# Performance work log

Measured on AMD Instinct MI355X. Metric: run time of the kernel, lower is better.

## Reference

```python
import jax, jax.numpy as jnp
import numpy as np

B, T = 4, 2048
OBS, ST = 512, 512
H, E = 8, 64

def setup_inputs() -> dict:
    key = jax.random.key(0)
    k1, k2, k3, k4, k5 = jax.random.split(key, 5)
    observe = jax.random.normal(k1, (B, T, OBS), dtype=jnp.float32)
    state = jax.random.normal(k2, (B, T, ST), dtype=jnp.float32)
    # nn.Linear weights (out, in) applied as x @ W.T; store transposed for einsum
    Wq = jax.random.normal(k3, (OBS, H * E), dtype=jnp.float32) * (1.0 / np.sqrt(OBS))
    Wk = jax.random.normal(k4, (ST, H * E), dtype=jnp.float32) * (1.0 / np.sqrt(ST))
    Wv = jax.random.normal(k5, (ST, H * E), dtype=jnp.float32) * (1.0 / np.sqrt(ST))
    merge_w = jnp.ones((1, H, E), dtype=jnp.float32)  # Merger weight, init fill_(1.0)
    return {"observe": observe, "state": state, "Wq": Wq, "Wk": Wk, "Wv": Wv, "merge_w": merge_w}

def reference(observe, state, Wq, Wk, Wv, merge_w):
    b, t, _ = observe.shape
    h, e = H, E
    scale = e ** 0.25
    q = (observe @ Wq).reshape(b, t, h, e).transpose(0, 2, 1, 3) / scale  # [b,h,t,e]
    k = (state @ Wk).reshape(b, t, h, e).transpose(0, 2, 1, 3) / scale
    v = (state @ Wv).reshape(b, t, h, e).transpose(0, 2, 1, 3)
    dot = jnp.einsum('bhqe,bhke->bhqk', q, k)  # [b,h,t,t]
    attn = jax.nn.softmax(dot, axis=-1)
    out = jnp.einsum('bhqk,bhke->bhqe', attn, v)  # [b,h,t,e]
    out = out.transpose(0, 2, 1, 3).reshape(b * t, h, e)  # [b*t,h,e]
    # Merger: softmax over head dim of learned weight, weighted head sum
    w = jax.nn.softmax(merge_w, axis=1)  # [1,h,e]
    return jnp.sum(w * out, axis=1)  # [b*t,e]
```

## Files before the change

kernel.cpp:

```cpp
#include <hip/hip_runtime.h>

#define B_ 4
#define T_ 2048
#define H_ 8
#define E_ 64
#define KDIM 512

typedef unsigned short ushort_t;
typedef __attribute__((ext_vector_type(4))) float f32x4;
typedef __attribute__((ext_vector_type(4))) int i32x4;
typedef __attribute__((ext_vector_type(8))) short s16x8;

#define QK_SCALE 0.42466043f

__device__ __forceinline__ ushort_t f2bf(float f) {
  unsigned u = __builtin_bit_cast(unsigned, f);
  u += 0x7fffu + ((u >> 16) & 1u);
  return (ushort_t)(u >> 16);
}
__device__ __forceinline__ unsigned pk2(float a, float b) {
  return (unsigned)f2bf(a) | ((unsigned)f2bf(b) << 16);
}
__device__ __forceinline__ unsigned pk2t(float a, float b) {
  return __builtin_amdgcn_perm(__builtin_bit_cast(unsigned, b),
                               __builtin_bit_cast(unsigned, a), 0x07060302u);
}
__device__ __forceinline__ float e2(float x) { return __builtin_amdgcn_exp2f(x); }
__device__ __forceinline__ void gl2lds16(const void* g, void* l) {
  __builtin_amdgcn_global_load_lds((const __attribute__((address_space(1))) unsigned*)g,
                                   (__attribute__((address_space(3))) unsigned*)l, 16, 0, 0);
}

__global__ void k_prep(const float* __restrict__ Wq, const float* __restrict__ Wk,
                       const float* __restrict__ Wv, ushort_t* __restrict__ wt) {
  __shared__ ushort_t tile[64][66];
  int z = blockIdx.z;
  const float* W = (z == 0) ? Wq : (z == 1 ? Wk : Wv);
  float scale = (z < 2) ? QK_SCALE : 1.0f;
  int k0 = blockIdx.y << 6, n0 = blockIdx.x << 6;
  int rr = threadIdx.x >> 6, cc = threadIdx.x & 63;
  for (int p = 0; p < 16; p++) {
    int kl = p * 4 + rr;
    tile[cc][kl] = f2bf(W[(size_t)(k0 + kl) * 512 + n0 + cc] * scale);
  }
  __syncthreads();
  int kp2 = threadIdx.x & 31, nr = threadIdx.x >> 5;
  unsigned* wt32 = (unsigned*)(wt + (size_t)z * 262144);
  for (int p = 0; p < 8; p++) {
    int nl = p * 8 + nr;
    unsigned val = (unsigned)tile[nl][kp2 * 2] | ((unsigned)tile[nl][kp2 * 2 + 1] << 16);
    wt32[(size_t)(n0 + nl) * 256 + (k0 >> 1) + kp2] = val;
  }
}

__global__ void k_wgt(const float* __restrict__ mw, float* __restrict__ wgt) {
  int e = threadIdx.x;
  float w[8], wmax = -1e30f;
  for (int h = 0; h < 8; h++) { w[h] = mw[h * 64 + e]; wmax = fmaxf(wmax, w[h]); }
  float wsum = 0.f;
  for (int h = 0; h < 8; h++) { w[h] = __expf(w[h] - wmax); wsum += w[h]; }
  float inv = 1.f / wsum;
  for (int h = 0; h < 8; h++) wgt[h * 64 + e] = w[h] * inv;
}

__global__ void k_cvt(const float* __restrict__ obs, const float* __restrict__ st,
                      unsigned* __restrict__ xo, unsigned* __restrict__ xs) {
  int which = blockIdx.y;
  const float* src = which ? st : obs;
  unsigned* dst = which ? xs : xo;
  size_t idx = (size_t)blockIdx.x * 256 + threadIdx.x;
  size_t base = idx * 8;
  float4 x0 = *(const float4*)(src + base);
  float4 x1 = *(const float4*)(src + base + 4);
  uint4 d;
  d.x = pk2(x0.x, x0.y);
  d.y = pk2(x0.z, x0.w);
  d.z = pk2(x1.x, x1.y);
  d.w = pk2(x1.z, x1.w);
  *(uint4*)(dst + idx * 4) = d;
}

__global__ __launch_bounds__(256, 3) void k_proj2(
    const ushort_t* __restrict__ xo, const ushort_t* __restrict__ xs,
    const ushort_t* __restrict__ wt,
    ushort_t* __restrict__ qo, ushort_t* __restrict__ ko, ushort_t* __restrict__ vto) {
  __shared__ __align__(16) ushort_t As[3][128 * 64];

  int id = blockIdx.x;
  int xcd = id & 7, nt = (id >> 3) & 3, ghi = id >> 5;
  int g = ghi * 8 + xcd;
  int which = g >> 6, mb = g & 63;
  int m0 = mb << 7, n0 = nt << 7;
  const ushort_t* X = (which == 0) ? xo : xs;
  const ushort_t* W = wt + which * 262144;

  int tid = threadIdx.x, wave = tid >> 6, lane = tid & 63;
  int l15 = lane & 15, quad = lane >> 4;
  int wm = wave & 1, wn = wave >> 1;

  f32x4 acc[4][4];
  for (int i = 0; i < 4; i++)
    for (int j = 0; j < 4; j++) acc[i][j] = (f32x4){0.f, 0.f, 0.f, 0.f};

  int arl = lane >> 3, ap = lane & 7;

#define STAGEA(buf, k0)                                                            \
  do {                                                                             \
    for (int ii = 0; ii < 4; ii++) {                                               \
      int r = wave * 32 + ii * 8 + arl;                                            \
      gl2lds16(X + (size_t)(m0 + r) * KDIM + (k0) + ((ap ^ (r & 7)) << 3),         \
               &As[buf][(wave * 32 + ii * 8) * 64]);                               \
    }                                                                              \
  } while (0)

  const ushort_t* wb[4];
  for (int j = 0; j < 4; j++)
    wb[j] = W + (size_t)(n0 + wn * 64 + j * 16 + l15) * KDIM + quad * 8;

  STAGEA(0, 0);
  STAGEA(1, 64);
  __builtin_amdgcn_s_waitcnt(0x0F74);
  __builtin_amdgcn_s_barrier();
  __builtin_amdgcn_sched_barrier(0);

#pragma unroll
  for (int kt = 0; kt < 8; kt++) {
    s16x8 b[2][4];
    for (int kc = 0; kc < 2; kc++)
      for (int j = 0; j < 4; j++) b[kc][j] = *(const s16x8*)(wb[j] + kc * 32);
    for (int j = 0; j < 4; j++) wb[j] += 64;
    if (kt < 6) STAGEA((kt + 2) % 3, (kt + 2) * 64);
    if (kt < 6) __builtin_amdgcn_s_waitcnt(0x0F74);
    else        __builtin_amdgcn_s_waitcnt(0x0F70);
    __builtin_amdgcn_sched_barrier(0);
    const ushort_t* asb = As[kt % 3];
    for (int kc = 0; kc < 2; kc++) {
      s16x8 a[4];
      for (int i = 0; i < 4; i++) {
        int mr = wm * 64 + i * 16 + l15;
        int pc = (kc * 4 + quad) ^ (l15 & 7);
        a[i] = *(const s16x8*)&asb[mr * 64 + pc * 8];
      }
      if (which == 2) {
        for (int i = 0; i < 4; i++)
          for (int j = 0; j < 4; j++)
            acc[i][j] = __builtin_amdgcn_mfma_f32_16x16x32_bf16(b[kc][j], a[i], acc[i][j], 0, 0, 0);
      } else {
        for (int i = 0; i < 4; i++)
          for (int j = 0; j < 4; j++)
            acc[i][j] = __builtin_amdgcn_mfma_f32_16x16x32_bf16(a[i], b[kc][j], acc[i][j], 0, 0, 0);
      }
    }
    if (kt < 7) {
      __builtin_amdgcn_s_barrier();
      __builtin_amdgcn_sched_barrier(0);
    }
  }
#undef STAGEA

  if (which != 2) {
    ushort_t* dst = (which == 0) ? qo : ko;
    for (int i = 0; i < 4; i++) {
      int grow = m0 + wm * 64 + i * 16 + quad * 4;
      for (int j = 0; j < 4; j++) {
        int gcol = n0 + wn * 64 + j * 16 + l15;
        int h = gcol >> 6, e = gcol & 63;
        for (int r = 0; r < 4; r++) {
          int row = grow + r;
          int bb = row >> 11, t = row & 2047;
          int bh = bb * H_ + h;
          dst[(((size_t)bh * T_ + t) << 6) + e] = f2bf(acc[i][j][r]);
        }
      }
    }
  } else {
    for (int i = 0; i < 4; i++) {
      int row = m0 + wm * 64 + i * 16 + l15;
      int bb = row >> 11, t = row & 2047;
      for (int j = 0; j < 4; j++) {
        for (int r = 0; r < 4; r++) {
          int gcol = n0 + wn * 64 + j * 16 + quad * 4 + r;
          int h = gcol >> 6, e = gcol & 63;
          int bh = bb * H_ + h;
          vto[((size_t)(bh << 6) + e) * T_ + t] = f2bf(acc[i][j][r]);
        }
      }
    }
  }
}

__global__ __launch_bounds__(256, 3) void k_proj(
    const float* __restrict__ obs, const float* __restrict__ st,
    const ushort_t* __restrict__ wt,
    ushort_t* __restrict__ qo, ushort_t* __restrict__ ko, ushort_t* __restrict__ vto) {
  __shared__ __align__(16) float As[2][128 * 32];

  int id = blockIdx.x;
  int xcd = id & 7, nt = (id >> 3) & 3, ghi = id >> 5;
  int g = ghi * 8 + xcd;
  int which = g >> 6, mb = g & 63;
  int m0 = mb << 7, n0 = nt << 7;
  const float* X = (which == 0) ? obs : st;
  const ushort_t* W = wt + which * 262144;

  int tid = threadIdx.x, wave = tid >> 6, lane = tid & 63;
  int l15 = lane & 15, quad = lane >> 4;
  int wm = wave & 1, wn = wave >> 1;

  f32x4 acc[4][4];
  for (int i = 0; i < 4; i++)
    for (int j = 0; j < 4; j++) acc[i][j] = (f32x4){0.f, 0.f, 0.f, 0.f};

  int arl = lane >> 3, ap = lane & 7;

#define STAGEA(buf, k0)                                                           \
  do {                                                                            \
    for (int ii = 0; ii < 4; ii++) {                                              \
      int r = wave * 32 + ii * 8 + arl;                                           \
      gl2lds16(X + (size_t)(m0 + r) * KDIM + (k0) + ((ap ^ (r & 7)) << 2),        \
               &As[buf][(wave * 32 + ii * 8) * 32]);                              \
    }                                                                             \
  } while (0)

  const ushort_t* wb[4];
  for (int j = 0; j < 4; j++)
    wb[j] = W + (size_t)(n0 + wn * 64 + j * 16 + l15) * KDIM + quad * 8;

  STAGEA(0, 0);
  __builtin_amdgcn_s_waitcnt(0x0F70);
  __syncthreads();

  for (int kt = 0; kt < 16; kt++) {
    s16x8 b[4];
    for (int j = 0; j < 4; j++) { b[j] = *(const s16x8*)wb[j]; wb[j] += 32; }
    if (kt < 15) STAGEA((kt + 1) & 1, kt * 32 + 32);
    const float* asb = As[kt & 1];
    s16x8 a[4];
    for (int i = 0; i < 4; i++) {
      int mr = wm * 64 + i * 16 + l15;
      int s = mr & 7;
      const float* rowp = &asb[mr * 32];
      float4 x0 = *(const float4*)&rowp[(((quad << 1)) ^ s) << 2];
      float4 x1 = *(const float4*)&rowp[(((quad << 1) | 1) ^ s) << 2];
      i32x4 d;
      d[0] = (int)pk2(x0.x, x0.y);
      d[1] = (int)pk2(x0.z, x0.w);
      d[2] = (int)pk2(x1.x, x1.y);
      d[3] = (int)pk2(x1.z, x1.w);
      a[i] = __builtin_bit_cast(s16x8, d);
    }
    if (which == 2) {
      for (int i = 0; i < 4; i++)
        for (int j = 0; j < 4; j++)
          acc[i][j] = __builtin_amdgcn_mfma_f32_16x16x32_bf16(b[j], a[i], acc[i][j], 0, 0, 0);
    } else {
      for (int i = 0; i < 4; i++)
        for (int j = 0; j < 4; j++)
          acc[i][j] = __builtin_amdgcn_mfma_f32_16x16x32_bf16(a[i], b[j], acc[i][j], 0, 0, 0);
    }
    __builtin_amdgcn_s_waitcnt(0x0F70);
    __syncthreads();
  }
#undef STAGEA

  if (which != 2) {
    ushort_t* dst = (which == 0) ? qo : ko;
    for (int i = 0; i < 4; i++) {
      int grow = m0 + wm * 64 + i * 16 + quad * 4;
      for (int j = 0; j < 4; j++) {
        int gcol = n0 + wn * 64 + j * 16 + l15;
        int h = gcol >> 6, e = gcol & 63;
        for (int r = 0; r < 4; r++) {
          int row = grow + r;
          int bb = row >> 11, t = row & 2047;
          int bh = bb * H_ + h;
          dst[(((size_t)bh * T_ + t) << 6) + e] = f2bf(acc[i][j][r]);
        }
      }
    }
  } else {
    for (int i = 0; i < 4; i++) {
      int row = m0 + wm * 64 + i * 16 + l15;
      int bb = row >> 11, t = row & 2047;
      for (int j = 0; j < 4; j++) {
        for (int r = 0; r < 4; r++) {
          int gcol = n0 + wn * 64 + j * 16 + quad * 4 + r;
          int h = gcol >> 6, e = gcol & 63;
          int bh = bb * H_ + h;
          vto[((size_t)(bh << 6) + e) * T_ + t] = f2bf(acc[i][j][r]);
        }
      }
    }
  }
}

union AttnSmem {
  struct { ushort_t ks[3][64 * 64]; ushort_t vs[3][64 * 64]; } st;
  struct { float ows[64 * 65]; float linv[64]; } ep;
};

__global__ __launch_bounds__(256, 2) void k_attn(
    const ushort_t* __restrict__ q, const ushort_t* __restrict__ k,
    const ushort_t* __restrict__ vt, const float* __restrict__ wgt,
    float* __restrict__ out) {
  __shared__ __align__(16) AttnSmem sm;

  int id = blockIdx.x;
  int bh = id & 31, qt = id >> 5;
  int tid = threadIdx.x, wave = tid >> 6, lane = tid & 63;
  int l15 = lane & 15, quad = lane >> 4;

  s16x8 qf[2][2];
  for (int qs = 0; qs < 2; qs++) {
    const ushort_t* qp =
        q + (((size_t)bh * T_ + qt * 128 + wave * 32 + qs * 16 + l15) << 6) + quad * 8;
    qf[qs][0] = *(const s16x8*)qp;
    qf[qs][1] = *(const s16x8*)(qp + 32);
  }
  int hh = bh & 7;
  float wgl = wgt[hh * 64 + lane];

  f32x4 o[2][4];
  for (int qs = 0; qs < 2; qs++)
    for (int j = 0; j < 4; j++) o[qs][j] = (f32x4){0.f, 0.f, 0.f, 0.f};
  f32x4 lacc[2] = {(f32x4){0.f, 0.f, 0.f, 0.f}, (f32x4){0.f, 0.f, 0.f, 0.f}};
  const s16x8 ones = {16256, 16256, 16256, 16256, 16256, 16256, 16256, 16256};

  int srl = lane >> 3, sp = lane & 7;
  const ushort_t* kbase = k + ((size_t)bh * T_ << 6);
  const ushort_t* vbase = vt + ((size_t)bh << 6) * T_;
  const ushort_t* kptr[2];
  const ushort_t* vptr[2];
  for (int ii = 0; ii < 2; ii++) {
    int r = wave * 16 + ii * 8 + srl;
    int gkey = (r & 32) + (((r >> 2) & 3) << 3) + (((r >> 4) & 1) << 2) + (r & 3);
    kptr[ii] = kbase + ((size_t)gkey << 6) + ((sp ^ (r & 7)) << 3);
    int e = r;
    vptr[ii] = vbase + (size_t)e * T_ + ((sp ^ (e & 7)) << 3);
  }

#define STAGE(buf)                                                         \
  do {                                                                     \
    for (int ii = 0; ii < 2; ii++) {                                       \
      gl2lds16(kptr[ii], &sm.st.ks[buf][(wave * 16 + ii * 8) * 64]);       \
      gl2lds16(vptr[ii], &sm.st.vs[buf][(wave * 16 + ii * 8) * 64]);       \
      kptr[ii] += 64 * 64;                                                 \
      vptr[ii] += 64;                                                      \
    }                                                                      \
  } while (0)

  STAGE(0);
  STAGE(1);
  __builtin_amdgcn_s_waitcnt(0x0F74);
  __builtin_amdgcn_s_barrier();
  __builtin_amdgcn_sched_barrier(0);

  int cur = 0, pre = 2;
  for (int kt = 0; kt < 32; kt++) {
    if (kt < 30) STAGE(pre);
    const ushort_t* ksb = &sm.st.ks[0][0] + cur * 4096;
    const ushort_t* vsb = &sm.st.vs[0][0] + cur * 4096;

    s16x8 bfr[2][2];
    for (int c = 0; c < 2; c++) {
      f32x4 s0[2], s1[2];
      for (int qs = 0; qs < 2; qs++) {
        s0[qs] = (f32x4){0.f, 0.f, 0.f, 0.f};
        s1[qs] = (f32x4){0.f, 0.f, 0.f, 0.f};
      }
      for (int kc = 0; kc < 2; kc++) {
        int pc = (kc * 4 + quad) ^ (l15 & 7);
        s16x8 k0f = *(const s16x8*)&ksb[(c * 32 + l15) * 64 + pc * 8];
        s16x8 k1f = *(const s16x8*)&ksb[(c * 32 + 16 + l15) * 64 + pc * 8];
        for (int qs = 0; qs < 2; qs++) {
          s0[qs] = __builtin_amdgcn_mfma_f32_16x16x32_bf16(k0f, qf[qs][kc], s0[qs], 0, 0, 0);
          s1[qs] = __builtin_amdgcn_mfma_f32_16x16x32_bf16(k1f, qf[qs][kc], s1[qs], 0, 0, 0);
        }
      }
      for (int qs = 0; qs < 2; qs++) {
        i32x4 d;
        d[0] = (int)pk2t(e2(s0[qs][0]), e2(s0[qs][1]));
        d[1] = (int)pk2t(e2(s0[qs][2]), e2(s0[qs][3]));
        d[2] = (int)pk2t(e2(s1[qs][0]), e2(s1[qs][1]));
        d[3] = (int)pk2t(e2(s1[qs][2]), e2(s1[qs][3]));
        bfr[qs][c] = __builtin_bit_cast(s16x8, d);
      }
    }

    for (int c = 0; c < 2; c++) {
      lacc[0] = __builtin_amdgcn_mfma_f32_16x16x32_bf16(ones, bfr[0][c], lacc[0], 0, 0, 0);
      lacc[1] = __builtin_amdgcn_mfma_f32_16x16x32_bf16(ones, bfr[1][c], lacc[1], 0, 0, 0);
      for (int et = 0; et < 4; et++) {
        int pc = (c * 4 + quad) ^ (l15 & 7);
        s16x8 vf = *(const s16x8*)&vsb[(et * 16 + l15) * 64 + pc * 8];
        o[0][et] = __builtin_amdgcn_mfma_f32_16x16x32_bf16(vf, bfr[0][c], o[0][et], 0, 0, 0);
        o[1][et] = __builtin_amdgcn_mfma_f32_16x16x32_bf16(vf, bfr[1][c], o[1][et], 0, 0, 0);
      }
    }

    if (kt < 30)       __builtin_amdgcn_s_waitcnt(0x0F74);
    else if (kt == 30) __builtin_amdgcn_s_waitcnt(0x0F70);
    if (kt < 31) {
      __builtin_amdgcn_s_barrier();
      __builtin_amdgcn_sched_barrier(0);
    }
    int nc = cur + 1; cur = (nc == 3) ? 0 : nc;
    int np = pre + 1; pre = (np == 3) ? 0 : np;
  }
#undef STAGE

  int bb = bh >> 3;
  for (int half = 0; half < 2; half++) {
    __syncthreads();
    if ((wave >> 1) == half) {
      int tl = (wave & 1) * 32;
      for (int qs = 0; qs < 2; qs++) {
        int row = tl + qs * 16 + l15;
        if (quad == 0) sm.ep.linv[row] = 1.f / lacc[qs][0];
        for (int et = 0; et < 4; et++)
          for (int r = 0; r < 4; r++)
            sm.ep.ows[row * 65 + et * 16 + quad * 4 + r] = o[qs][et][r];
      }
    }
    __syncthreads();
    for (int i = 0; i < 16; i++) {
      int row = wave * 16 + i;
      int gt = qt * 128 + half * 64 + row;
      float val = sm.ep.ows[row * 65 + lane] * sm.ep.linv[row] * wgl;
      atomicAdd(&out[(((size_t)bb * T_ + gt) << 6) + lane], val);
    }
  }
}

extern "C" void kernel_launch(void* const* d_in, const int* in_sizes, int n_in,
                              void* d_out, int out_size, void* d_ws, size_t ws_size,
                              hipStream_t stream) {
  const float* obs = (const float*)d_in[0];
  const float* st  = (const float*)d_in[1];
  const float* Wq  = (const float*)d_in[2];
  const float* Wk  = (const float*)d_in[3];
  const float* Wv  = (const float*)d_in[4];
  const float* mw  = (const float*)d_in[5];

  const size_t WS_NEEDED = 27262976;
  const size_t WS_BIG    = 44040192;
  char* ws = (char*)d_ws;
  ushort_t* wt  = (ushort_t*)ws;
  float*    wgt = (float*)(ws + 1572864u);
  ushort_t* qo  = (ushort_t*)(ws + 2097152u);
  ushort_t* ko  = (ushort_t*)(ws + 10485760u);
  ushort_t* vto = (ushort_t*)(ws + 18874368u);
  ushort_t* xo  = (ushort_t*)(ws + 27262976u);
  ushort_t* xs  = (ushort_t*)(ws + 35651584u);
  float*    out = (float*)d_out;

  hipMemsetAsync(d_out, 0, (size_t)out_size * sizeof(float), stream);
  if (ws_size < WS_NEEDED) return;

  hipLaunchKernelGGL(k_prep, dim3(8, 8, 3), dim3(256), 0, stream, Wq, Wk, Wv, wt);
  hipLaunchKernelGGL(k_wgt,  dim3(1),       dim3(64),  0, stream, mw, wgt);
  if (ws_size >= WS_BIG) {
    hipLaunchKernelGGL(k_cvt,   dim3(2048, 2), dim3(256), 0, stream, obs, st,
                       (unsigned*)xo, (unsigned*)xs);
    hipLaunchKernelGGL(k_proj2, dim3(768),     dim3(256), 0, stream, xo, xs, wt, qo, ko, vto);
  } else {
    hipLaunchKernelGGL(k_proj,  dim3(768),     dim3(256), 0, stream, obs, st, wt, qo, ko, vto);
  }
  hipLaunchKernelGGL(k_attn, dim3(512), dim3(256), 0, stream, qo, ko, vto, wgt, out);
}
```

Before: 186.3 us.

## Halve attention query tile, double grid, and prefetch projection weights a step ahead

The attention kernel now handles 64 query rows per block (16 per wave) instead of 128, which doubles the grid to 1024 blocks and raises the launch-bounds occupancy hint to 3 blocks per CU. The epilogue becomes a single pass with no two-half loop. Separately, the projection GEMM double-buffers its global weight-fragment loads in registers one k-step ahead, with adjusted waitcnt values. The trade-off is more parallelism against twice the K/V tile loads from L2/HBM per query row.

New measurement: 226.7 us. 1.22x slower.

```diff
diff --git a/kernel.cpp b/kernel.cpp
--- a/kernel.cpp
+++ b/kernel.cpp
@@ -117,7 +117,12 @@
   for (int j = 0; j < 4; j++)
     wb[j] = W + (size_t)(n0 + wn * 64 + j * 16 + l15) * KDIM + quad * 8;
 
+  s16x8 bA[2][4], bB[2][4];
+
   STAGEA(0, 0);
+  for (int kc = 0; kc < 2; kc++)
+    for (int j = 0; j < 4; j++) bA[kc][j] = *(const s16x8*)(wb[j] + kc * 32);
+  for (int j = 0; j < 4; j++) wb[j] += 64;
   STAGEA(1, 64);
   __builtin_amdgcn_s_waitcnt(0x0F74);
   __builtin_amdgcn_s_barrier();
@@ -125,13 +130,17 @@
 
 #pragma unroll
   for (int kt = 0; kt < 8; kt++) {
-    s16x8 b[2][4];
-    for (int kc = 0; kc < 2; kc++)
-      for (int j = 0; j < 4; j++) b[kc][j] = *(const s16x8*)(wb[j] + kc * 32);
-    for (int j = 0; j < 4; j++) wb[j] += 64;
+    s16x8 (&bc)[2][4] = (kt & 1) ? bB : bA;
+    s16x8 (&bn)[2][4] = (kt & 1) ? bA : bB;
+    if (kt < 7) {
+      for (int kc = 0; kc < 2; kc++)
+        for (int j = 0; j < 4; j++) bn[kc][j] = *(const s16x8*)(wb[j] + kc * 32);
+      for (int j = 0; j < 4; j++) wb[j] += 64;
+    }
     if (kt < 6) STAGEA((kt + 2) % 3, (kt + 2) * 64);
-    if (kt < 6) __builtin_amdgcn_s_waitcnt(0x0F74);
-    else        __builtin_amdgcn_s_waitcnt(0x0F70);
+    if (kt < 6)      __builtin_amdgcn_s_waitcnt(0x0F7C);
+    else if (kt == 6) __builtin_amdgcn_s_waitcnt(0x0F78);
+    else              __builtin_amdgcn_s_waitcnt(0x0F70);
     __builtin_amdgcn_sched_barrier(0);
     const ushort_t* asb = As[kt % 3];
     for (int kc = 0; kc < 2; kc++) {
@@ -144,11 +153,11 @@
       if (which == 2) {
         for (int i = 0; i < 4; i++)
           for (int j = 0; j < 4; j++)
-            acc[i][j] = __builtin_amdgcn_mfma_f32_16x16x32_bf16(b[kc][j], a[i], acc[i][j], 0, 0, 0);
+            acc[i][j] = __builtin_amdgcn_mfma_f32_16x16x32_bf16(bc[kc][j], a[i], acc[i][j], 0, 0, 0);
       } else {
         for (int i = 0; i < 4; i++)
           for (int j = 0; j < 4; j++)
-            acc[i][j] = __builtin_amdgcn_mfma_f32_16x16x32_bf16(a[i], b[kc][j], acc[i][j], 0, 0, 0);
+            acc[i][j] = __builtin_amdgcn_mfma_f32_16x16x32_bf16(a[i], bc[kc][j], acc[i][j], 0, 0, 0);
       }
     }
     if (kt < 7) {
@@ -299,7 +308,7 @@
   struct { float ows[64 * 65]; float linv[64]; } ep;
 };
 
-__global__ __launch_bounds__(256, 2) void k_attn(
+__global__ __launch_bounds__(256, 3) void k_attn(
     const ushort_t* __restrict__ q, const ushort_t* __restrict__ k,
     const ushort_t* __restrict__ vt, const float* __restrict__ wgt,
     float* __restrict__ out) {
@@ -310,20 +319,19 @@
   int tid = threadIdx.x, wave = tid >> 6, lane = tid & 63;
   int l15 = lane & 15, quad = lane >> 4;
 
-  s16x8 qf[2][2];
-  for (int qs = 0; qs < 2; qs++) {
+  s16x8 qf[2];
+  {
     const ushort_t* qp =
-        q + (((size_t)bh * T_ + qt * 128 + wave * 32 + qs * 16 + l15) << 6) + quad * 8;
-    qf[qs][0] = *(const s16x8*)qp;
-    qf[qs][1] = *(const s16x8*)(qp + 32);
+        q + (((size_t)bh * T_ + qt * 64 + wave * 16 + l15) << 6) + quad * 8;
+    qf[0] = *(const s16x8*)qp;
+    qf[1] = *(const s16x8*)(qp + 32);
   }
   int hh = bh & 7;
   float wgl = wgt[hh * 64 + lane];
 
-  f32x4 o[2][4];
-  for (int qs = 0; qs < 2; qs++)
-    for (int j = 0; j < 4; j++) o[qs][j] = (f32x4){0.f, 0.f, 0.f, 0.f};
-  f32x4 lacc[2] = {(f32x4){0.f, 0.f, 0.f, 0.f}, (f32x4){0.f, 0.f, 0.f, 0.f}};
+  f32x4 o[4];
+  for (int j = 0; j < 4; j++) o[j] = (f32x4){0.f, 0.f, 0.f, 0.f};
+  f32x4 lacc = (f32x4){0.f, 0.f, 0.f, 0.f};
   const s16x8 ones = {16256, 16256, 16256, 16256, 16256, 16256, 16256, 16256};
 
   int srl = lane >> 3, sp = lane & 7;
@@ -361,40 +369,31 @@
     const ushort_t* ksb = &sm.st.ks[0][0] + cur * 4096;
     const ushort_t* vsb = &sm.st.vs[0][0] + cur * 4096;
 
-    s16x8 bfr[2][2];
+    s16x8 bfr[2];
     for (int c = 0; c < 2; c++) {
-      f32x4 s0[2], s1[2];
-      for (int qs = 0; qs < 2; qs++) {
-        s0[qs] = (f32x4){0.f, 0.f, 0.f, 0.f};
-        s1[qs] = (f32x4){0.f, 0.f, 0.f, 0.f};
-      }
+      f32x4 s0 = (f32x4){0.f, 0.f, 0.f, 0.f};
+      f32x4 s1 = (f32x4){0.f, 0.f, 0.f, 0.f};
       for (int kc = 0; kc < 2; kc++) {
         int pc = (kc * 4 + quad) ^ (l15 & 7);
         s16x8 k0f = *(const s16x8*)&ksb[(c * 32 + l15) * 64 + pc * 8];
         s16x8 k1f = *(const s16x8*)&ksb[(c * 32 + 16 + l15) * 64 + pc * 8];
-        for (int qs = 0; qs < 2; qs++) {
-          s0[qs] = __builtin_amdgcn_mfma_f32_16x16x32_bf16(k0f, qf[qs][kc], s0[qs], 0, 0, 0);
-          s1[qs] = __builtin_amdgcn_mfma_f32_16x16x32_bf16(k1f, qf[qs][kc], s1[qs], 0, 0, 0);
-        }
-      }
-      for (int qs = 0; qs < 2; qs++) {
-        i32x4 d;
-        d[0] = (int)pk2t(e2(s0[qs][0]), e2(s0[qs][1]));
-        d[1] = (int)pk2t(e2(s0[qs][2]), e2(s0[qs][3]));
-        d[2] = (int)pk2t(e2(s1[qs][0]), e2(s1[qs][1]));
-        d[3] = (int)pk2t(e2(s1[qs][2]), e2(s1[qs][3]));
-        bfr[qs][c] = __builtin_bit_cast(s16x8, d);
-      }
+        s0 = __builtin_amdgcn_mfma_f32_16x16x32_bf16(k0f, qf[kc], s0, 0, 0, 0);
+        s1 = __builtin_amdgcn_mfma_f32_16x16x32_bf16(k1f, qf[kc], s1, 0, 0, 0);
+      }
+      i32x4 d;
+      d[0] = (int)pk2t(e2(s0[0]), e2(s0[1]));
+      d[1] = (int)pk2t(e2(s0[2]), e2(s0[3]));
+      d[2] = (int)pk2t(e2(s1[0]), e2(s1[1]));
+      d[3] = (int)pk2t(e2(s1[2]), e2(s1[3]));
+      bfr[c] = __builtin_bit_cast(s16x8, d);
     }
 
     for (int c = 0; c < 2; c++) {
-      lacc[0] = __builtin_amdgcn_mfma_f32_16x16x32_bf16(ones, bfr[0][c], lacc[0], 0, 0, 0);
-      lacc[1] = __builtin_amdgcn_mfma_f32_16x16x32_bf16(ones, bfr[1][c], lacc[1], 0, 0, 0);
+      lacc = __builtin_amdgcn_mfma_f32_16x16x32_bf16(ones, bfr[c], lacc, 0, 0, 0);
       for (int et = 0; et < 4; et++) {
         int pc = (c * 4 + quad) ^ (l15 & 7);
         s16x8 vf = *(const s16x8*)&vsb[(et * 16 + l15) * 64 + pc * 8];
-        o[0][et] = __builtin_amdgcn_mfma_f32_16x16x32_bf16(vf, bfr[0][c], o[0][et], 0, 0, 0);
-        o[1][et] = __builtin_amdgcn_mfma_f32_16x16x32_bf16(vf, bfr[1][c], o[1][et], 0, 0, 0);
+        o[et] = __builtin_amdgcn_mfma_f32_16x16x32_bf16(vf, bfr[c], o[et], 0, 0, 0);
       }
     }
 
@@ -410,22 +409,16 @@
 #undef STAGE
 
   int bb = bh >> 3;
-  for (int half = 0; half < 2; half++) {
-    __syncthreads();
-    if ((wave >> 1) == half) {
-      int tl = (wave & 1) * 32;
-      for (int qs = 0; qs < 2; qs++) {
-        int row = tl + qs * 16 + l15;
-        if (quad == 0) sm.ep.linv[row] = 1.f / lacc[qs][0];
-        for (int et = 0; et < 4; et++)
-          for (int r = 0; r < 4; r++)
-            sm.ep.ows[row * 65 + et * 16 + quad * 4 + r] = o[qs][et][r];
-      }
-    }
-    __syncthreads();
+  __syncthreads();
+  {
+    int row0 = wave * 16;
+    if (quad == 0) sm.ep.linv[row0 + l15] = 1.f / lacc[0];
+    for (int et = 0; et < 4; et++)
+      for (int r = 0; r < 4; r++)
+        sm.ep.ows[(row0 + l15) * 65 + et * 16 + quad * 4 + r] = o[et][r];
     for (int i = 0; i < 16; i++) {
-      int row = wave * 16 + i;
-      int gt = qt * 128 + half * 64 + row;
+      int row = row0 + i;
+      int gt = qt * 64 + row;
       float val = sm.ep.ows[row * 65 + lane] * sm.ep.linv[row] * wgl;
       atomicAdd(&out[(((size_t)bb * T_ + gt) << 6) + lane], val);
     }
@@ -466,5 +459,5 @@
   } else {
     hipLaunchKernelGGL(k_proj,  dim3(768),     dim3(256), 0, stream, obs, st, wt, qo, ko, vto);
   }
-  hipLaunchKernelGGL(k_attn, dim3(512), dim3(256), 0, stream, qo, ko, vto, wgt, out);
-}
+  hipLaunchKernelGGL(k_attn, dim3(1024), dim3(256), 0, stream, qo, ko, vto, wgt, out);
+}
```
